# Kernel optimization log

Hardware: AMD Instinct MI355X
Metric: run time of the kernel (lower is better)

## Reference

```python
import jax, jax.numpy as jnp
import numpy as np

HEAD_DIM = 64
EPS = 1e-06


def yat_dense(x, kernel, bias):
    # YatDense (nmn): y = (x.W)^2 / (||x - w||^2 + eps) * alpha_scale + b
    dot = x @ kernel                                  # [..., F]
    x_sq = jnp.sum(x * x, axis=-1, keepdims=True)     # [..., 1]
    w_sq = jnp.sum(kernel * kernel, axis=0)           # [F]
    dist = x_sq + w_sq - 2.0 * dot                    # squared euclidean distance
    y = (dot * dot) / (dist + EPS)
    feats = kernel.shape[1]
    scale = np.sqrt(feats) / np.log1p(feats)          # alpha=1 scaling
    return y * jnp.asarray(scale, x.dtype) + bias


def apply_rope(q, k):
    # q,k: [B,H,T,D]; interleaved-pair rotation, base 10000 (dim=HEAD_DIM)
    B, H, T, D = q.shape
    half = D // 2
    pos = jnp.arange(T, dtype=jnp.float32)
    freqs = 10000.0 ** (-jnp.arange(half, dtype=jnp.float32) / half)
    ang = pos[:, None] * freqs[None, :]               # [T, half]
    sin = jnp.sin(ang)[None, None, :, :, None]        # [1,1,T,half,1]
    cos = jnp.cos(ang)[None, None, :, :, None]

    def rot(t):
        ts = t.reshape(B, H, T, half, 2)
        t0, t1 = ts[..., 0:1], ts[..., 1:2]
        out = jnp.concatenate([t0 * cos - t1 * sin, t1 * cos + t0 * sin], axis=-1)
        return out.reshape(B, H, T, D)

    return rot(q), rot(k)


def setup_inputs() -> dict:
    key = jax.random.key(0)
    B, T, C, H = 2, 2048, 1024, 16
    k1, k2, k3, k4, k5 = jax.random.split(key, 5)
    x = jax.random.normal(k1, (B, T, C), dtype=jnp.float32)
    # causal mask, broadcast over batch
    mask = jnp.broadcast_to(jnp.tril(jnp.ones((T, T), dtype=bool))[None], (B, T, T))
    s = 1.0 / np.sqrt(C)
    w_attn = jax.random.normal(k2, (C, 3 * C), dtype=jnp.float32) * s
    b_attn = jnp.zeros((3 * C,), dtype=jnp.float32)
    w_proj = jax.random.normal(k3, (C, C), dtype=jnp.float32) * s
    b_proj = jnp.zeros((C,), dtype=jnp.float32)
    return {"x": x, "mask": mask, "w_attn": w_attn, "b_attn": b_attn,
            "w_proj": w_proj, "b_proj": b_proj}


def reference(x, mask, w_attn, b_attn, w_proj, b_proj):
    B, T, C = x.shape
    H = C // HEAD_DIM
    qkv = yat_dense(x, w_attn, b_attn)                     # [B,T,3C]
    qkv = qkv.reshape(B, T, 3, H, HEAD_DIM)
    q, k, v = jnp.moveaxis(qkv, 2, 0)                      # each [B,T,H,hd]
    q = jnp.swapaxes(q, 1, 2)                              # [B,H,T,hd]
    k = jnp.swapaxes(k, 1, 2)
    v = jnp.swapaxes(v, 1, 2)
    q, k = apply_rope(q, k)
    scale = jnp.asarray(np.sqrt(HEAD_DIM), x.dtype)
    attn = jnp.einsum('bhqd,bhkd->bhqk', q, k) / scale     # [B,H,T,T]
    neg = jnp.finfo(x.dtype).min
    attn = jnp.where(mask[:, None, :, :], attn, neg)
    attn = jax.nn.softmax(attn, axis=-1)
    out = jnp.einsum('bhqk,bhkd->bhqd', attn, v)           # [B,H,T,hd]
    out = jnp.swapaxes(out, 1, 2).reshape(B, T, C)
    return yat_dense(out, w_proj, b_proj)
```

## Files before the change

### kernel.cpp

```cpp
#include <hip/hip_runtime.h>
#include <hip/hip_bf16.h>
#include <cmath>

#define BB 2
#define TT 2048
#define CC 1024
#define HH 16
#define DD 64
#define ROWS (BB*TT)
#define N1 (3*CC)
#define EPS 1e-6f

using short8 = __attribute__((ext_vector_type(8))) short;
using f32x4  = __attribute__((ext_vector_type(4))) float;

__device__ __forceinline__ void gl_lds16(const __hip_bfloat16* g, unsigned short* l) {
    __builtin_amdgcn_global_load_lds(
        (const __attribute__((address_space(1))) unsigned int*)(g),
        (__attribute__((address_space(3))) unsigned int*)(l), 16, 0, 0);
}

__device__ __forceinline__ unsigned int bf16pair(float a, float b) {
    __hip_bfloat16 ha = (__hip_bfloat16)a, hb = (__hip_bfloat16)b;
    unsigned short ua = *(unsigned short*)&ha, ub = *(unsigned short*)&hb;
    return (unsigned int)ua | ((unsigned int)ub << 16);
}

__global__ void rope_rowsq(const float* __restrict__ X, float* __restrict__ xsq,
                           __hip_bfloat16* __restrict__ Xb, float* __restrict__ osq,
                           float* __restrict__ rope,
                           float* __restrict__ wsqa, float* __restrict__ wsqp) {
    int blk = blockIdx.x;
    int t = threadIdx.x;
    if (blk >= ROWS) {
        int idx = (blk - ROWS) * 256 + t;
        if (idx < N1) wsqa[idx] = 0.f;
        if (idx < CC) wsqp[idx] = 0.f;
        if (idx < TT * 32) {
            int tt = idx >> 5, i = idx & 31;
            double freq = pow(10000.0, -(double)i / 32.0);
            float ang = (float)tt * (float)freq;
            rope[idx * 2 + 0] = cosf(ang);
            rope[idx * 2 + 1] = sinf(ang);
        }
        return;
    }
    int row = blk;
    const float* xr = X + (size_t)row * CC;
    __hip_bfloat16* br = Xb + (size_t)row * CC;
    float p = 0.f;
#pragma unroll
    for (int i = 0; i < 4; ++i) {
        float v = xr[t + i * 256];
        p += v * v;
        br[t + i * 256] = (__hip_bfloat16)v;
    }
    __shared__ float s[256];
    s[t] = p;
    __syncthreads();
    for (int off = 128; off > 0; off >>= 1) {
        if (t < off) s[t] += s[t + off];
        __syncthreads();
    }
    if (t == 0) { xsq[row] = s[0]; osq[row] = 0.f; }
}

__global__ void transpose2(const float* __restrict__ Wa, __hip_bfloat16* __restrict__ WaT,
                           float* __restrict__ wsqa,
                           const float* __restrict__ Wp, __hip_bfloat16* __restrict__ WpT,
                           float* __restrict__ wsqp) {
    const float* W; __hip_bfloat16* Wt; float* wsq; int N;
    if (blockIdx.z == 0) { W = Wa; Wt = WaT; wsq = wsqa; N = N1; }
    else { if (blockIdx.x >= 16) return; W = Wp; Wt = WpT; wsq = wsqp; N = CC; }
    const int K = CC;
    __shared__ unsigned short tile[64][65];
    int n0 = blockIdx.x * 64, k0 = blockIdx.y * 64;
    int c = threadIdx.x & 63, rg = threadIdx.x >> 6;
    float part = 0.f;
#pragma unroll
    for (int rr = 0; rr < 16; ++rr) {
        int r = rg + rr * 4;
        float f = W[(size_t)(k0 + r) * N + n0 + c];
        __hip_bfloat16 h = (__hip_bfloat16)f;
        tile[r][c] = *(unsigned short*)&h;
        part += f * f;
    }
    atomicAdd(&wsq[n0 + c], part);
    __syncthreads();
#pragma unroll
    for (int rr = 0; rr < 16; ++rr) {
        int r = rg + rr * 4;
        unsigned short u = tile[c][r];
        Wt[(size_t)(n0 + r) * K + k0 + c] = *(__hip_bfloat16*)&u;
    }
}

__global__ __launch_bounds__(256) void yat_gemm_qkv(
    const __hip_bfloat16* __restrict__ A,
    const __hip_bfloat16* __restrict__ Bt,
    const float* __restrict__ xsq, const float* __restrict__ wsq,
    const float* __restrict__ bias, const float* __restrict__ rope,
    __hip_bfloat16* __restrict__ Qb, __hip_bfloat16* __restrict__ Kb,
    __hip_bfloat16* __restrict__ Vb, float scale) {
    const int K = CC, N = N1;
    __shared__ __align__(16) unsigned short As0[128 * 32], As1[128 * 32];
    __shared__ __align__(16) unsigned short Bs0[128 * 32], Bs1[128 * 32];
    int tid = threadIdx.x;
    int wave = tid >> 6, lane = tid & 63, quad = lane >> 4, l16 = lane & 15;
    int wr = wave >> 1, wc = wave & 1;
    int m0 = blockIdx.y * 128, n0 = blockIdx.x * 128;

    f32x4 acc[4][4];
#pragma unroll
    for (int mt = 0; mt < 4; ++mt)
#pragma unroll
        for (int nt = 0; nt < 4; ++nt) acc[mt][nt] = f32x4{0.f, 0.f, 0.f, 0.f};

    int srow = lane >> 2, soff = (lane & 3) << 3;
    for (int k0 = 0; k0 < K; k0 += 64) {
        __syncthreads();
#pragma unroll
        for (int i = 0; i < 2; ++i) {
            int rowc = (wave * 2 + i) * 16;
            const __hip_bfloat16* ap = A + (size_t)(m0 + rowc + srow) * K + k0 + soff;
            gl_lds16(ap,      As0 + rowc * 32);
            gl_lds16(ap + 32, As1 + rowc * 32);
            const __hip_bfloat16* bp = Bt + (size_t)(n0 + rowc + srow) * K + k0 + soff;
            gl_lds16(bp,      Bs0 + rowc * 32);
            gl_lds16(bp + 32, Bs1 + rowc * 32);
        }
        __syncthreads();
#pragma unroll
        for (int h = 0; h < 2; ++h) {
            const unsigned short* Ah = h ? As1 : As0;
            const unsigned short* Bh = h ? Bs1 : Bs0;
            short8 af[4], bf[4];
#pragma unroll
            for (int mt = 0; mt < 4; ++mt)
                af[mt] = *(const short8*)(Ah + (wr * 64 + mt * 16 + l16) * 32 + quad * 8);
#pragma unroll
            for (int nt = 0; nt < 4; ++nt)
                bf[nt] = *(const short8*)(Bh + (wc * 64 + nt * 16 + l16) * 32 + quad * 8);
#pragma unroll
            for (int mt = 0; mt < 4; ++mt)
#pragma unroll
                for (int nt = 0; nt < 4; ++nt)
                    acc[mt][nt] = __builtin_amdgcn_mfma_f32_16x16x32_bf16(af[mt], bf[nt], acc[mt][nt], 0, 0, 0);
        }
    }
    const float QSC = 0.125f * 1.44269504f;
    int mb = m0 + wr * 64 + quad * 4;
    int cbase = n0 + wc * 64;
    int sec = n0 >> 10;
    if (sec == 2) {
#pragma unroll
        for (int nt = 0; nt < 4; ++nt) {
            int col = cbase + nt * 16 + l16;
            float wq = wsq[col], bs = bias[col];
            int h = (col & 1023) >> 6, d = col & 63;
#pragma unroll
            for (int mt = 0; mt < 4; ++mt) {
#pragma unroll
                for (int r = 0; r < 4; ++r) {
                    int row = mb + mt * 16 + r;
                    float dot = acc[mt][nt][r];
                    float dist = xsq[row] + wq - 2.f * dot + EPS;
                    float y = dot * dot / dist * scale + bs;
                    int t = row & (TT - 1), bI = row >> 11;
                    Vb[(((size_t)bI * HH + h) * TT + t) * DD + d] = (__hip_bfloat16)y;
                }
            }
        }
    } else {
        __hip_bfloat16* dst = sec ? Kb : Qb;
        float sc = sec ? 1.f : QSC;
#pragma unroll
        for (int nt = 0; nt < 4; ++nt) {
            int col = cbase + nt * 16 + l16;
            float wq = wsq[col], bs = bias[col];
            int h = (col & 1023) >> 6, d = col & 63;
            int odd = l16 & 1;
#pragma unroll
            for (int mt = 0; mt < 4; ++mt) {
#pragma unroll
                for (int r = 0; r < 4; ++r) {
                    int row = mb + mt * 16 + r;
                    float dot = acc[mt][nt][r];
                    float dist = xsq[row] + wq - 2.f * dot + EPS;
                    float y = dot * dot / dist * scale + bs;
                    float yp = __shfl_xor(y, 1, 64);
                    int t = row & (TT - 1), bI = row >> 11;
                    const float* rp = rope + (size_t)t * 64 + (d & 62);
                    float cs = rp[0] * sc, sn = rp[1] * sc;
                    float o = odd ? (y * cs + yp * sn) : (y * cs - yp * sn);
                    dst[(((size_t)bI * HH + h) * TT + t) * DD + d] = (__hip_bfloat16)o;
                }
            }
        }
    }
}

__global__ __launch_bounds__(256) void vtrans(const unsigned short* __restrict__ Vb,
                                              __hip_bfloat16* __restrict__ Vtb) {
    int bh = blockIdx.y, t0 = blockIdx.x * 64, tid = threadIdx.x;
    __shared__ unsigned short vt[64][72];
    int r = tid >> 2, g = (tid & 3) * 16;
    const unsigned short* src = Vb + ((size_t)bh * TT + t0 + r) * DD + g;
    *(uint4*)&vt[r][g]     = *(const uint4*)src;
    *(uint4*)&vt[r][g + 8] = *(const uint4*)(src + 8);
    __syncthreads();
    union U8 { uint4 v; unsigned short s[8]; };
#pragma unroll
    for (int p = 0; p < 2; ++p) {
        int d = (tid >> 3) + p * 32, tl = (tid & 7) * 8;
        U8 w;
#pragma unroll
        for (int j = 0; j < 8; ++j) w.s[j] = vt[tl + j][d];
        *(uint4*)(Vtb + ((size_t)bh * DD + d) * TT + t0 + tl) = w.v;
    }
}

__global__ __launch_bounds__(256, 3) void attn_mfma6(
    const __hip_bfloat16* __restrict__ Qb, const __hip_bfloat16* __restrict__ Kb,
    const __hip_bfloat16* __restrict__ Vtb,
    __hip_bfloat16* __restrict__ out, float* __restrict__ osq) {
    int i = blockIdx.x;
    int xcd = i & 7;
    int r0 = i >> 3;
    int bh = xcd + 8 * (r0 & 3);
    int rr = r0 >> 2;
    int v = rr & 7, s2 = rr >> 3;
    int qblk = (s2 == 0) ? v : (s2 == 1) ? (15 - v) : (s2 == 2) ? (16 + v) : (31 - v);
    int b = bh >> 4, h = bh & 15;
    int tid = threadIdx.x;
    int wave = tid >> 6, lane = tid & 63, quad = lane >> 4, l16 = lane & 15;

    __shared__ __align__(16) unsigned short Ks[2][64 * 32];
    __shared__ __align__(16) unsigned short Vs[2][64 * 32];
    __shared__ __align__(16) unsigned short Ps[4][16 * 72];
    unsigned short* pp = &Ps[wave][0];

    const __hip_bfloat16* Qbase = Qb + (size_t)bh * TT * DD;
    const __hip_bfloat16* Kbase = Kb + (size_t)bh * TT * DD;
    const __hip_bfloat16* Vbase = Vtb + (size_t)bh * DD * TT;

    int qw = qblk * 64 + wave * 16;
    short8 qf0, qf1;
    {
        const __hip_bfloat16* qr = Qbase + (size_t)(qw + l16) * DD + quad * 8;
        qf0 = *(const short8*)(qr);
        qf1 = *(const short8*)(qr + 32);
    }
    short8 ones8;
#pragma unroll
    for (int u = 0; u < 8; ++u) ones8[u] = (short)0x3F80;

    f32x4 acc_o[4];
#pragma unroll
    for (int mt = 0; mt < 4; ++mt) acc_o[mt] = f32x4{0.f, 0.f, 0.f, 0.f};
    f32x4 acc_l = {0.f, 0.f, 0.f, 0.f};

    int srow = lane >> 2;
    int soff = (lane & 3) * 8;
    int q_g = qw + l16;

    for (int kt = 0; kt <= qblk; ++kt) {
        int k0 = kt * 64;
        __syncthreads();
        gl_lds16(Kbase + (size_t)(k0 + wave * 16 + srow) * DD + soff,      &Ks[0][wave * 512]);
        gl_lds16(Kbase + (size_t)(k0 + wave * 16 + srow) * DD + 32 + soff, &Ks[1][wave * 512]);
        gl_lds16(Vbase + (size_t)(wave * 16 + srow) * TT + k0 + soff,      &Vs[0][wave * 512]);
        gl_lds16(Vbase + (size_t)(wave * 16 + srow) * TT + k0 + 32 + soff, &Vs[1][wave * 512]);
        __syncthreads();

        f32x4 accs[4];
#pragma unroll
        for (int mt = 0; mt < 4; ++mt) {
            short8 kf0 = *(const short8*)(&Ks[0][(mt * 16 + l16) * 32 + quad * 8]);
            short8 kf1 = *(const short8*)(&Ks[1][(mt * 16 + l16) * 32 + quad * 8]);
            f32x4 z = {0.f, 0.f, 0.f, 0.f};
            z = __builtin_amdgcn_mfma_f32_16x16x32_bf16(kf0, qf0, z, 0, 0, 0);
            accs[mt] = __builtin_amdgcn_mfma_f32_16x16x32_bf16(kf1, qf1, z, 0, 0, 0);
        }
        int limit = (kt == qblk) ? q_g : 0x7FFFFFFF;
#pragma unroll
        for (int mt = 0; mt < 4; ++mt) {
            int keyb = k0 + mt * 16 + quad * 4;
            float p0 = exp2f(accs[mt][0]);
            float p1 = exp2f(accs[mt][1]);
            float p2 = exp2f(accs[mt][2]);
            float p3 = exp2f(accs[mt][3]);
            p0 = (keyb + 0 <= limit) ? p0 : 0.f;
            p1 = (keyb + 1 <= limit) ? p1 : 0.f;
            p2 = (keyb + 2 <= limit) ? p2 : 0.f;
            p3 = (keyb + 3 <= limit) ? p3 : 0.f;
            uint2 w2;
            w2.x = bf16pair(p0, p1);
            w2.y = bf16pair(p2, p3);
            *(uint2*)(pp + l16 * 72 + mt * 16 + quad * 4) = w2;
        }
        short8 pf0 = *(const short8*)(pp + l16 * 72 + quad * 8);
        short8 pf1 = *(const short8*)(pp + l16 * 72 + 32 + quad * 8);
#pragma unroll
        for (int mt = 0; mt < 4; ++mt) {
            short8 vf0 = *(const short8*)(&Vs[0][(mt * 16 + l16) * 32 + quad * 8]);
            short8 vf1 = *(const short8*)(&Vs[1][(mt * 16 + l16) * 32 + quad * 8]);
            acc_o[mt] = __builtin_amdgcn_mfma_f32_16x16x32_bf16(vf0, pf0, acc_o[mt], 0, 0, 0);
            acc_o[mt] = __builtin_amdgcn_mfma_f32_16x16x32_bf16(vf1, pf1, acc_o[mt], 0, 0, 0);
        }
        acc_l = __builtin_amdgcn_mfma_f32_16x16x32_bf16(ones8, pf0, acc_l, 0, 0, 0);
        acc_l = __builtin_amdgcn_mfma_f32_16x16x32_bf16(ones8, pf1, acc_l, 0, 0, 0);
    }
    float inv = 1.f / acc_l[0];
    float part = 0.f;
#pragma unroll
    for (int mt = 0; mt < 4; ++mt) {
        float o0 = acc_o[mt][0] * inv;
        float o1 = acc_o[mt][1] * inv;
        float o2 = acc_o[mt][2] * inv;
        float o3 = acc_o[mt][3] * inv;
        part += o0 * o0 + o1 * o1 + o2 * o2 + o3 * o3;
        uint2 w2;
        w2.x = bf16pair(o0, o1);
        w2.y = bf16pair(o2, o3);
        *(uint2*)(pp + l16 * 72 + mt * 16 + quad * 4) = w2;
    }
    part += __shfl_xor(part, 16, 64);
    part += __shfl_xor(part, 32, 64);
    if (quad == 0) atomicAdd(&osq[(size_t)b * TT + qw + l16], part);
    int rw = lane >> 2, cg = lane & 3;
    uint4 o0 = *(const uint4*)(pp + rw * 72 + cg * 16);
    uint4 o1 = *(const uint4*)(pp + rw * 72 + cg * 16 + 8);
    __hip_bfloat16* orow = out + (size_t)(b * TT + qw + rw) * CC + h * DD + cg * 16;
    *(uint4*)(orow) = o0;
    *(uint4*)(orow + 8) = o1;
}

template<int TM, int TN, typename OutT>
__global__ __launch_bounds__(256) void yat_gemm_bk64(
    const __hip_bfloat16* __restrict__ A,
    const __hip_bfloat16* __restrict__ Bt,
    const float* __restrict__ xsq, const float* __restrict__ wsq,
    const float* __restrict__ bias, OutT* __restrict__ C,
    int M, int N, int K, float scale) {
    constexpr int MT = TM / 32;
    constexpr int NT = TN / 32;
    constexpr int IA = TM / 64;
    constexpr int IB = TN / 64;
    __shared__ __align__(16) unsigned short As0[TM * 32];
    __shared__ __align__(16) unsigned short As1[TM * 32];
    __shared__ __align__(16) unsigned short Bs0[TN * 32];
    __shared__ __align__(16) unsigned short Bs1[TN * 32];
    int tid = threadIdx.x;
    int wave = tid >> 6, lane = tid & 63, quad = lane >> 4, l16 = lane & 15;
    int wr = wave >> 1, wc = wave & 1;
    int m0 = blockIdx.y * TM, n0 = blockIdx.x * TN;

    f32x4 acc[MT][NT];
#pragma unroll
    for (int mt = 0; mt < MT; ++mt)
#pragma unroll
        for (int nt = 0; nt < NT; ++nt) acc[mt][nt] = f32x4{0.f, 0.f, 0.f, 0.f};

    int srow = lane >> 2, soff = (lane & 3) << 3;
    for (int k0 = 0; k0 < K; k0 += 64) {
        __syncthreads();
#pragma unroll
        for (int i = 0; i < IA; ++i) {
            int rowc = (wave * IA + i) * 16;
            const __hip_bfloat16* ap = A + (size_t)(m0 + rowc + srow) * K + k0 + soff;
            gl_lds16(ap,      As0 + rowc * 32);
            gl_lds16(ap + 32, As1 + rowc * 32);
        }
#pragma unroll
        for (int i = 0; i < IB; ++i) {
            int rowc = (wave * IB + i) * 16;
            const __hip_bfloat16* bp = Bt + (size_t)(n0 + rowc + srow) * K + k0 + soff;
            gl_lds16(bp,      Bs0 + rowc * 32);
            gl_lds16(bp + 32, Bs1 + rowc * 32);
        }
        __syncthreads();
#pragma unroll
        for (int h = 0; h < 2; ++h) {
            const unsigned short* Ah = h ? As1 : As0;
            const unsigned short* Bh = h ? Bs1 : Bs0;
            short8 af[MT], bf[NT];
#pragma unroll
            for (int mt = 0; mt < MT; ++mt)
                af[mt] = *(const short8*)(Ah + (wr * (TM / 2) + mt * 16 + l16) * 32 + quad * 8);
#pragma unroll
            for (int nt = 0; nt < NT; ++nt)
                bf[nt] = *(const short8*)(Bh + (wc * (TN / 2) + nt * 16 + l16) * 32 + quad * 8);
#pragma unroll
            for (int mt = 0; mt < MT; ++mt)
#pragma unroll
                for (int nt = 0; nt < NT; ++nt)
                    acc[mt][nt] = __builtin_amdgcn_mfma_f32_16x16x32_bf16(af[mt], bf[nt], acc[mt][nt], 0, 0, 0);
        }
    }
    int mb = m0 + wr * (TM / 2) + quad * 4;
#pragma unroll
    for (int nt = 0; nt < NT; ++nt) {
        int col = n0 + wc * (TN / 2) + nt * 16 + l16;
        float wq = wsq[col];
        float bs = bias[col];
#pragma unroll
        for (int mt = 0; mt < MT; ++mt) {
#pragma unroll
            for (int r = 0; r < 4; ++r) {
                int row = mb + mt * 16 + r;
                float dot = acc[mt][nt][r];
                float dist = xsq[row] + wq - 2.f * dot + EPS;
                C[(size_t)row * N + col] = (OutT)(dot * dot / dist * scale + bs);
            }
        }
    }
}

extern "C" void kernel_launch(void* const* d_in, const int* in_sizes, int n_in,
                              void* d_out, int out_size, void* d_ws, size_t ws_size,
                              hipStream_t stream) {
    const float* x      = (const float*)d_in[0];
    const float* w_attn = (const float*)d_in[2];
    const float* b_attn = (const float*)d_in[3];
    const float* w_proj = (const float*)d_in[4];
    const float* b_proj = (const float*)d_in[5];
    float* out = (float*)d_out;

    char* ws = (char*)d_ws;
    __hip_bfloat16* xbf  = (__hip_bfloat16*)(ws + 0);
    __hip_bfloat16* aout = (__hip_bfloat16*)(ws + 8388608);
    __hip_bfloat16* watT = (__hip_bfloat16*)(ws + 16777216);
    __hip_bfloat16* wpT  = (__hip_bfloat16*)(ws + 23068672);
    float*          rope = (float*)(ws + 25165824);
    float*          xsq  = (float*)(ws + 25690112);
    float*          osq  = (float*)(ws + 25706496);
    float*          wsqa = (float*)(ws + 25722880);
    float*          wsqp = (float*)(ws + 25735168);
    __hip_bfloat16* Qb   = (__hip_bfloat16*)(ws + 25739264);
    __hip_bfloat16* Kb   = (__hip_bfloat16*)(ws + 34127872);
    __hip_bfloat16* Vb   = (__hip_bfloat16*)(ws + 42516480);
    __hip_bfloat16* Vtb  = (__hip_bfloat16*)(ws + 50905088);

    float scale1 = (float)(sqrt(3072.0) / log1p(3072.0));
    float scale2 = (float)(sqrt(1024.0) / log1p(1024.0));

    rope_rowsq<<<ROWS + 256, 256, 0, stream>>>(x, xsq, xbf, osq, rope, wsqa, wsqp);
    transpose2<<<dim3(48, 16, 2), 256, 0, stream>>>(w_attn, watT, wsqa, w_proj, wpT, wsqp);
    yat_gemm_qkv<<<dim3(N1 / 128, ROWS / 128), 256, 0, stream>>>(
        xbf, watT, xsq, wsqa, b_attn, rope, Qb, Kb, Vb, scale1);
    vtrans<<<dim3(TT / 64, BB * HH), 256, 0, stream>>>((const unsigned short*)Vb, Vtb);
    attn_mfma6<<<1024, 256, 0, stream>>>(Qb, Kb, Vtb, aout, osq);
    yat_gemm_bk64<128, 64, float><<<dim3(CC / 64, ROWS / 128), 256, 0, stream>>>(
        aout, wpT, osq, wsqp, b_proj, out, ROWS, CC, CC, scale2);
}
```

Baseline: 246.8 us.

## Double-buffer attention K/V, pair causal blocks, move RoPE out of QKV GEMM

The attention kernel now double-buffers its K/V LDS tiles so the next tile's loads overlap the current tile's MFMAs. Causal query blocks are paired per workgroup (768 blocks) to balance work. RoPE is moved out of the QKV GEMM epilogue: K is rotated in place in the V-transpose kernel and Q is rotated when loaded in attention. The row-norm reduction switches to wave shuffles, and the output projection uses smaller 64x64 tiles. The cost is extra K read/write traffic, more LDS per block, and a different occupancy and scheduling balance.

```diff
diff --git a/kernel.cpp b/kernel.cpp
--- a/kernel.cpp
+++ b/kernel.cpp
@@ -26,10 +26,15 @@
     return (unsigned int)ua | ((unsigned int)ub << 16);
 }
 
-__global__ void rope_rowsq(const float* __restrict__ X, float* __restrict__ xsq,
-                           __hip_bfloat16* __restrict__ Xb, float* __restrict__ osq,
-                           float* __restrict__ rope,
-                           float* __restrict__ wsqa, float* __restrict__ wsqp) {
+__device__ __forceinline__ float bf2f(unsigned short u) {
+    unsigned int v = (unsigned int)u << 16;
+    return *(float*)&v;
+}
+
+__global__ void aux_rowsq(const float* __restrict__ X, float* __restrict__ xsq,
+                          __hip_bfloat16* __restrict__ Xb, float* __restrict__ osq,
+                          float* __restrict__ rope,
+                          float* __restrict__ wsqa, float* __restrict__ wsqp) {
     int blk = blockIdx.x;
     int t = threadIdx.x;
     if (blk >= ROWS) {
@@ -55,14 +60,12 @@
         p += v * v;
         br[t + i * 256] = (__hip_bfloat16)v;
     }
-    __shared__ float s[256];
-    s[t] = p;
+#pragma unroll
+    for (int off = 32; off > 0; off >>= 1) p += __shfl_xor(p, off, 64);
+    __shared__ float s4[4];
+    if ((t & 63) == 0) s4[t >> 6] = p;
     __syncthreads();
-    for (int off = 128; off > 0; off >>= 1) {
-        if (t < off) s[t] += s[t + off];
-        __syncthreads();
-    }
-    if (t == 0) { xsq[row] = s[0]; osq[row] = 0.f; }
+    if (t == 0) { xsq[row] = s4[0] + s4[1] + s4[2] + s4[3]; osq[row] = 0.f; }
 }
 
 __global__ void transpose2(const float* __restrict__ Wa, __hip_bfloat16* __restrict__ WaT,
@@ -95,14 +98,14 @@
     }
 }
 
-__global__ __launch_bounds__(256) void yat_gemm_qkv(
+__global__ __launch_bounds__(256) void yat_gemm_qkv2(
     const __hip_bfloat16* __restrict__ A,
     const __hip_bfloat16* __restrict__ Bt,
     const float* __restrict__ xsq, const float* __restrict__ wsq,
-    const float* __restrict__ bias, const float* __restrict__ rope,
+    const float* __restrict__ bias,
     __hip_bfloat16* __restrict__ Qb, __hip_bfloat16* __restrict__ Kb,
     __hip_bfloat16* __restrict__ Vb, float scale) {
-    const int K = CC, N = N1;
+    const int K = CC;
     __shared__ __align__(16) unsigned short As0[128 * 32], As1[128 * 32];
     __shared__ __align__(16) unsigned short Bs0[128 * 32], Bs1[128 * 32];
     int tid = threadIdx.x;
@@ -148,95 +151,84 @@
                     acc[mt][nt] = __builtin_amdgcn_mfma_f32_16x16x32_bf16(af[mt], bf[nt], acc[mt][nt], 0, 0, 0);
         }
     }
-    const float QSC = 0.125f * 1.44269504f;
     int mb = m0 + wr * 64 + quad * 4;
-    int cbase = n0 + wc * 64;
-    int sec = n0 >> 10;
-    if (sec == 2) {
-#pragma unroll
-        for (int nt = 0; nt < 4; ++nt) {
-            int col = cbase + nt * 16 + l16;
-            float wq = wsq[col], bs = bias[col];
-            int h = (col & 1023) >> 6, d = col & 63;
-#pragma unroll
-            for (int mt = 0; mt < 4; ++mt) {
-#pragma unroll
-                for (int r = 0; r < 4; ++r) {
-                    int row = mb + mt * 16 + r;
-                    float dot = acc[mt][nt][r];
-                    float dist = xsq[row] + wq - 2.f * dot + EPS;
-                    float y = dot * dot / dist * scale + bs;
-                    int t = row & (TT - 1), bI = row >> 11;
-                    Vb[(((size_t)bI * HH + h) * TT + t) * DD + d] = (__hip_bfloat16)y;
-                }
-            }
-        }
-    } else {
-        __hip_bfloat16* dst = sec ? Kb : Qb;
-        float sc = sec ? 1.f : QSC;
-#pragma unroll
-        for (int nt = 0; nt < 4; ++nt) {
-            int col = cbase + nt * 16 + l16;
-            float wq = wsq[col], bs = bias[col];
-            int h = (col & 1023) >> 6, d = col & 63;
-            int odd = l16 & 1;
-#pragma unroll
-            for (int mt = 0; mt < 4; ++mt) {
-#pragma unroll
-                for (int r = 0; r < 4; ++r) {
-                    int row = mb + mt * 16 + r;
-                    float dot = acc[mt][nt][r];
-                    float dist = xsq[row] + wq - 2.f * dot + EPS;
-                    float y = dot * dot / dist * scale + bs;
-                    float yp = __shfl_xor(y, 1, 64);
-                    int t = row & (TT - 1), bI = row >> 11;
-                    const float* rp = rope + (size_t)t * 64 + (d & 62);
-                    float cs = rp[0] * sc, sn = rp[1] * sc;
-                    float o = odd ? (y * cs + yp * sn) : (y * cs - yp * sn);
-                    dst[(((size_t)bI * HH + h) * TT + t) * DD + d] = (__hip_bfloat16)o;
-                }
-            }
-        }
-    }
-}
-
-__global__ __launch_bounds__(256) void vtrans(const unsigned short* __restrict__ Vb,
-                                              __hip_bfloat16* __restrict__ Vtb) {
+#pragma unroll
+    for (int nt = 0; nt < 4; ++nt) {
+        int col = n0 + wc * 64 + nt * 16 + l16;
+        float wq = wsq[col], bs = bias[col];
+        int sec = col >> 10, cc2 = col & 1023;
+        int h = cc2 >> 6, d = cc2 & 63;
+        __hip_bfloat16* dst = (sec == 0) ? Qb : ((sec == 1) ? Kb : Vb);
+#pragma unroll
+        for (int mt = 0; mt < 4; ++mt) {
+#pragma unroll
+            for (int r = 0; r < 4; ++r) {
+                int row = mb + mt * 16 + r;
+                float dot = acc[mt][nt][r];
+                float dist = xsq[row] + wq - 2.f * dot + EPS;
+                float y = dot * dot / dist * scale + bs;
+                int t = row & (TT - 1), bI = row >> 11;
+                dst[(((size_t)bI * HH + h) * TT + t) * DD + d] = (__hip_bfloat16)y;
+            }
+        }
+    }
+}
+
+__global__ __launch_bounds__(256) void ropek_vtrans(
+    unsigned short* __restrict__ Kb, const unsigned short* __restrict__ Vb,
+    __hip_bfloat16* __restrict__ Vtb, const float* __restrict__ rope) {
     int bh = blockIdx.y, t0 = blockIdx.x * 64, tid = threadIdx.x;
     __shared__ unsigned short vt[64][72];
-    int r = tid >> 2, g = (tid & 3) * 16;
-    const unsigned short* src = Vb + ((size_t)bh * TT + t0 + r) * DD + g;
-    *(uint4*)&vt[r][g]     = *(const uint4*)src;
-    *(uint4*)&vt[r][g + 8] = *(const uint4*)(src + 8);
+    int r = tid >> 2, g = tid & 3;
+    const unsigned short* src = Vb + ((size_t)bh * TT + t0 + r) * DD + g * 16;
+    *(uint4*)&vt[r][g * 16]     = *(const uint4*)src;
+    *(uint4*)&vt[r][g * 16 + 8] = *(const uint4*)(src + 8);
+    {
+        int t = t0 + r;
+        unsigned short* kp = Kb + ((size_t)bh * TT + t) * DD + g * 16;
+        union U8 { uint4 v; unsigned short s[8]; } k0v, k1v, o0, o1;
+        k0v.v = *(const uint4*)kp;
+        k1v.v = *(const uint4*)(kp + 8);
+        const float* rp = rope + (size_t)t * 64 + g * 16;
+#pragma unroll
+        for (int u = 0; u < 8; ++u) {
+            float c = rp[2 * u], sn = rp[2 * u + 1];
+            unsigned short ev = (u < 4) ? k0v.s[2 * u]     : k1v.s[2 * u - 8];
+            unsigned short ov = (u < 4) ? k0v.s[2 * u + 1] : k1v.s[2 * u - 7];
+            float f0 = bf2f(ev), f1 = bf2f(ov);
+            unsigned int pr = bf16pair(f0 * c - f1 * sn, f1 * c + f0 * sn);
+            if (u < 4) ((unsigned int*)&o0)[u] = pr;
+            else       ((unsigned int*)&o1)[u - 4] = pr;
+        }
+        *(uint4*)kp = o0.v;
+        *(uint4*)(kp + 8) = o1.v;
+    }
     __syncthreads();
-    union U8 { uint4 v; unsigned short s[8]; };
+    union U8b { uint4 v; unsigned short s[8]; };
 #pragma unroll
     for (int p = 0; p < 2; ++p) {
         int d = (tid >> 3) + p * 32, tl = (tid & 7) * 8;
-        U8 w;
+        U8b w;
 #pragma unroll
         for (int j = 0; j < 8; ++j) w.s[j] = vt[tl + j][d];
         *(uint4*)(Vtb + ((size_t)bh * DD + d) * TT + t0 + tl) = w.v;
     }
 }
 
-__global__ __launch_bounds__(256, 3) void attn_mfma6(
+__global__ __launch_bounds__(256, 3) void attn_mfma8(
     const __hip_bfloat16* __restrict__ Qb, const __hip_bfloat16* __restrict__ Kb,
-    const __hip_bfloat16* __restrict__ Vtb,
+    const __hip_bfloat16* __restrict__ Vtb, const float* __restrict__ rope,
     __hip_bfloat16* __restrict__ out, float* __restrict__ osq) {
+    const float QSC = 0.125f * 1.44269504f;
     int i = blockIdx.x;
-    int xcd = i & 7;
-    int r0 = i >> 3;
-    int bh = xcd + 8 * (r0 & 3);
-    int rr = r0 >> 2;
-    int v = rr & 7, s2 = rr >> 3;
-    int qblk = (s2 == 0) ? v : (s2 == 1) ? (15 - v) : (s2 == 2) ? (16 + v) : (31 - v);
+    int xcd = i & 7, jj = (i >> 3) & 3, s = i >> 5;
+    int bh = xcd + 8 * jj;
     int b = bh >> 4, h = bh & 15;
     int tid = threadIdx.x;
     int wave = tid >> 6, lane = tid & 63, quad = lane >> 4, l16 = lane & 15;
 
-    __shared__ __align__(16) unsigned short Ks[2][64 * 32];
-    __shared__ __align__(16) unsigned short Vs[2][64 * 32];
+    __shared__ __align__(16) unsigned short Ks[2][2][64 * 32];
+    __shared__ __align__(16) unsigned short Vs[2][2][64 * 32];
     __shared__ __align__(16) unsigned short Ps[4][16 * 72];
     unsigned short* pp = &Ps[wave][0];
 
@@ -244,96 +236,125 @@
     const __hip_bfloat16* Kbase = Kb + (size_t)bh * TT * DD;
     const __hip_bfloat16* Vbase = Vtb + (size_t)bh * DD * TT;
 
-    int qw = qblk * 64 + wave * 16;
-    short8 qf0, qf1;
-    {
-        const __hip_bfloat16* qr = Qbase + (size_t)(qw + l16) * DD + quad * 8;
-        qf0 = *(const short8*)(qr);
-        qf1 = *(const short8*)(qr + 32);
-    }
+    int srow = lane >> 2, soff = (lane & 3) * 8;
     short8 ones8;
 #pragma unroll
     for (int u = 0; u < 8; ++u) ones8[u] = (short)0x3F80;
 
-    f32x4 acc_o[4];
-#pragma unroll
-    for (int mt = 0; mt < 4; ++mt) acc_o[mt] = f32x4{0.f, 0.f, 0.f, 0.f};
-    f32x4 acc_l = {0.f, 0.f, 0.f, 0.f};
-
-    int srow = lane >> 2;
-    int soff = (lane & 3) * 8;
-    int q_g = qw + l16;
-
-    for (int kt = 0; kt <= qblk; ++kt) {
-        int k0 = kt * 64;
+    int u0, u1, nunits;
+    if (s < 8)       { u0 = s;      u1 = 15 - s; nunits = 2; }
+    else if (s < 16) { u0 = s + 8;  u1 = 0;      nunits = 1; }
+    else             { u0 = 47 - s; u1 = 0;      nunits = 1; }
+
+    for (int un = 0; un < nunits; ++un) {
+        int qblk = un ? u1 : u0;
+        int qw = qblk * 64 + wave * 16;
+        short8 qf0, qf1;
+        {
+            int t = qw + l16;
+            const unsigned short* qr = (const unsigned short*)(Qbase + (size_t)t * DD) + quad * 8;
+            union S8 { short8 v; unsigned short s[8]; } r0, r1, o0v, o1v;
+            r0.v = *(const short8*)qr;
+            r1.v = *(const short8*)(qr + 32);
+            const float* rpa = rope + (size_t)t * 64 + quad * 8;
+            const float* rpb = rpa + 32;
+#pragma unroll
+            for (int u = 0; u < 4; ++u) {
+                float c = rpa[2 * u] * QSC, sn = rpa[2 * u + 1] * QSC;
+                float e = bf2f(r0.s[2 * u]), o = bf2f(r0.s[2 * u + 1]);
+                ((unsigned int*)&o0v)[u] = bf16pair(e * c - o * sn, o * c + e * sn);
+                float c2 = rpb[2 * u] * QSC, sn2 = rpb[2 * u + 1] * QSC;
+                float e2 = bf2f(r1.s[2 * u]), o2 = bf2f(r1.s[2 * u + 1]);
+                ((unsigned int*)&o1v)[u] = bf16pair(e2 * c2 - o2 * sn2, o2 * c2 + e2 * sn2);
+            }
+            qf0 = o0v.v;
+            qf1 = o1v.v;
+        }
+        f32x4 acc_o[4];
+#pragma unroll
+        for (int mt = 0; mt < 4; ++mt) acc_o[mt] = f32x4{0.f, 0.f, 0.f, 0.f};
+        f32x4 acc_l = {0.f, 0.f, 0.f, 0.f};
+        int q_g = qw + l16;
+
         __syncthreads();
-        gl_lds16(Kbase + (size_t)(k0 + wave * 16 + srow) * DD + soff,      &Ks[0][wave * 512]);
-        gl_lds16(Kbase + (size_t)(k0 + wave * 16 + srow) * DD + 32 + soff, &Ks[1][wave * 512]);
-        gl_lds16(Vbase + (size_t)(wave * 16 + srow) * TT + k0 + soff,      &Vs[0][wave * 512]);
-        gl_lds16(Vbase + (size_t)(wave * 16 + srow) * TT + k0 + 32 + soff, &Vs[1][wave * 512]);
-        __syncthreads();
-
-        f32x4 accs[4];
+        gl_lds16(Kbase + (size_t)(wave * 16 + srow) * DD + soff,      &Ks[0][0][wave * 512]);
+        gl_lds16(Kbase + (size_t)(wave * 16 + srow) * DD + 32 + soff, &Ks[0][1][wave * 512]);
+        gl_lds16(Vbase + (size_t)(wave * 16 + srow) * TT + soff,      &Vs[0][0][wave * 512]);
+        gl_lds16(Vbase + (size_t)(wave * 16 + srow) * TT + 32 + soff, &Vs[0][1][wave * 512]);
+
+        for (int kt = 0; kt <= qblk; ++kt) {
+            int cur = kt & 1;
+            int k0 = kt * 64;
+            __syncthreads();
+            if (kt < qblk) {
+                int nb = cur ^ 1, kn = k0 + 64;
+                gl_lds16(Kbase + (size_t)(kn + wave * 16 + srow) * DD + soff,      &Ks[nb][0][wave * 512]);
+                gl_lds16(Kbase + (size_t)(kn + wave * 16 + srow) * DD + 32 + soff, &Ks[nb][1][wave * 512]);
+                gl_lds16(Vbase + (size_t)(wave * 16 + srow) * TT + kn + soff,      &Vs[nb][0][wave * 512]);
+                gl_lds16(Vbase + (size_t)(wave * 16 + srow) * TT + kn + 32 + soff, &Vs[nb][1][wave * 512]);
+            }
+            f32x4 accs[4];
+#pragma unroll
+            for (int mt = 0; mt < 4; ++mt) {
+                short8 kf0 = *(const short8*)(&Ks[cur][0][(mt * 16 + l16) * 32 + quad * 8]);
+                short8 kf1 = *(const short8*)(&Ks[cur][1][(mt * 16 + l16) * 32 + quad * 8]);
+                f32x4 z = {0.f, 0.f, 0.f, 0.f};
+                z = __builtin_amdgcn_mfma_f32_16x16x32_bf16(kf0, qf0, z, 0, 0, 0);
+                accs[mt] = __builtin_amdgcn_mfma_f32_16x16x32_bf16(kf1, qf1, z, 0, 0, 0);
+            }
+            int limit = (kt == qblk) ? q_g : 0x7FFFFFFF;
+#pragma unroll
+            for (int mt = 0; mt < 4; ++mt) {
+                int keyb = k0 + mt * 16 + quad * 4;
+                float p0 = exp2f(accs[mt][0]);
+                float p1 = exp2f(accs[mt][1]);
+                float p2 = exp2f(accs[mt][2]);
+                float p3 = exp2f(accs[mt][3]);
+                p0 = (keyb + 0 <= limit) ? p0 : 0.f;
+                p1 = (keyb + 1 <= limit) ? p1 : 0.f;
+                p2 = (keyb + 2 <= limit) ? p2 : 0.f;
+                p3 = (keyb + 3 <= limit) ? p3 : 0.f;
+                uint2 w2;
+                w2.x = bf16pair(p0, p1);
+                w2.y = bf16pair(p2, p3);
+                *(uint2*)(pp + l16 * 72 + mt * 16 + quad * 4) = w2;
+            }
+            short8 pf0 = *(const short8*)(pp + l16 * 72 + quad * 8);
+            short8 pf1 = *(const short8*)(pp + l16 * 72 + 32 + quad * 8);
+#pragma unroll
+            for (int mt = 0; mt < 4; ++mt) {
+                short8 vf0 = *(const short8*)(&Vs[cur][0][(mt * 16 + l16) * 32 + quad * 8]);
+                short8 vf1 = *(const short8*)(&Vs[cur][1][(mt * 16 + l16) * 32 + quad * 8]);
+                acc_o[mt] = __builtin_amdgcn_mfma_f32_16x16x32_bf16(vf0, pf0, acc_o[mt], 0, 0, 0);
+                acc_o[mt] = __builtin_amdgcn_mfma_f32_16x16x32_bf16(vf1, pf1, acc_o[mt], 0, 0, 0);
+            }
+            acc_l = __builtin_amdgcn_mfma_f32_16x16x32_bf16(ones8, pf0, acc_l, 0, 0, 0);
+            acc_l = __builtin_amdgcn_mfma_f32_16x16x32_bf16(ones8, pf1, acc_l, 0, 0, 0);
+        }
+        float inv = 1.f / acc_l[0];
+        float part = 0.f;
 #pragma unroll
         for (int mt = 0; mt < 4; ++mt) {
-            short8 kf0 = *(const short8*)(&Ks[0][(mt * 16 + l16) * 32 + quad * 8]);
-            short8 kf1 = *(const short8*)(&Ks[1][(mt * 16 + l16) * 32 + quad * 8]);
-            f32x4 z = {0.f, 0.f, 0.f, 0.f};
-            z = __builtin_amdgcn_mfma_f32_16x16x32_bf16(kf0, qf0, z, 0, 0, 0);
-            accs[mt] = __builtin_amdgcn_mfma_f32_16x16x32_bf16(kf1, qf1, z, 0, 0, 0);
-        }
-        int limit = (kt == qblk) ? q_g : 0x7FFFFFFF;
-#pragma unroll
-        for (int mt = 0; mt < 4; ++mt) {
-            int keyb = k0 + mt * 16 + quad * 4;
-            float p0 = exp2f(accs[mt][0]);
-            float p1 = exp2f(accs[mt][1]);
-            float p2 = exp2f(accs[mt][2]);
-            float p3 = exp2f(accs[mt][3]);
-            p0 = (keyb + 0 <= limit) ? p0 : 0.f;
-            p1 = (keyb + 1 <= limit) ? p1 : 0.f;
-            p2 = (keyb + 2 <= limit) ? p2 : 0.f;
-            p3 = (keyb + 3 <= limit) ? p3 : 0.f;
+            float o0 = acc_o[mt][0] * inv;
+            float o1 = acc_o[mt][1] * inv;
+            float o2 = acc_o[mt][2] * inv;
+            float o3 = acc_o[mt][3] * inv;
+            part += o0 * o0 + o1 * o1 + o2 * o2 + o3 * o3;
             uint2 w2;
-            w2.x = bf16pair(p0, p1);
-            w2.y = bf16pair(p2, p3);
+            w2.x = bf16pair(o0, o1);
+            w2.y = bf16pair(o2, o3);
             *(uint2*)(pp + l16 * 72 + mt * 16 + quad * 4) = w2;
         }
-        short8 pf0 = *(const short8*)(pp + l16 * 72 + quad * 8);
-        short8 pf1 = *(const short8*)(pp + l16 * 72 + 32 + quad * 8);
-#pragma unroll
-        for (int mt = 0; mt < 4; ++mt) {
-            short8 vf0 = *(const short8*)(&Vs[0][(mt * 16 + l16) * 32 + quad * 8]);
-            short8 vf1 = *(const short8*)(&Vs[1][(mt * 16 + l16) * 32 + quad * 8]);
-            acc_o[mt] = __builtin_amdgcn_mfma_f32_16x16x32_bf16(vf0, pf0, acc_o[mt], 0, 0, 0);
-            acc_o[mt] = __builtin_amdgcn_mfma_f32_16x16x32_bf16(vf1, pf1, acc_o[mt], 0, 0, 0);
-        }
-        acc_l = __builtin_amdgcn_mfma_f32_16x16x32_bf16(ones8, pf0, acc_l, 0, 0, 0);
-        acc_l = __builtin_amdgcn_mfma_f32_16x16x32_bf16(ones8, pf1, acc_l, 0, 0, 0);
-    }
-    float inv = 1.f / acc_l[0];
-    float part = 0.f;
-#pragma unroll
-    for (int mt = 0; mt < 4; ++mt) {
-        float o0 = acc_o[mt][0] * inv;
-        float o1 = acc_o[mt][1] * inv;
-        float o2 = acc_o[mt][2] * inv;
-        float o3 = acc_o[mt][3] * inv;
-        part += o0 * o0 + o1 * o1 + o2 * o2 + o3 * o3;
-        uint2 w2;
-        w2.x = bf16pair(o0, o1);
-        w2.y = bf16pair(o2, o3);
-        *(uint2*)(pp + l16 * 72 + mt * 16 + quad * 4) = w2;
-    }
-    part += __shfl_xor(part, 16, 64);
-    part += __shfl_xor(part, 32, 64);
-    if (quad == 0) atomicAdd(&osq[(size_t)b * TT + qw + l16], part);
-    int rw = lane >> 2, cg = lane & 3;
-    uint4 o0 = *(const uint4*)(pp + rw * 72 + cg * 16);
-    uint4 o1 = *(const uint4*)(pp + rw * 72 + cg * 16 + 8);
-    __hip_bfloat16* orow = out + (size_t)(b * TT + qw + rw) * CC + h * DD + cg * 16;
-    *(uint4*)(orow) = o0;
-    *(uint4*)(orow + 8) = o1;
+        part += __shfl_xor(part, 16, 64);
+        part += __shfl_xor(part, 32, 64);
+        if (quad == 0) atomicAdd(&osq[(size_t)b * TT + qw + l16], part);
+        int rw = lane >> 2, cg = lane & 3;
+        uint4 o0 = *(const uint4*)(pp + rw * 72 + cg * 16);
+        uint4 o1 = *(const uint4*)(pp + rw * 72 + cg * 16 + 8);
+        __hip_bfloat16* orow = out + (size_t)(b * TT + qw + rw) * CC + h * DD + cg * 16;
+        *(uint4*)(orow) = o0;
+        *(uint4*)(orow + 8) = o1;
+    }
 }
 
 template<int TM, int TN, typename OutT>
@@ -445,12 +466,13 @@
     float scale1 = (float)(sqrt(3072.0) / log1p(3072.0));
     float scale2 = (float)(sqrt(1024.0) / log1p(1024.0));
 
-    rope_rowsq<<<ROWS + 256, 256, 0, stream>>>(x, xsq, xbf, osq, rope, wsqa, wsqp);
+    aux_rowsq<<<ROWS + 256, 256, 0, stream>>>(x, xsq, xbf, osq, rope, wsqa, wsqp);
     transpose2<<<dim3(48, 16, 2), 256, 0, stream>>>(w_attn, watT, wsqa, w_proj, wpT, wsqp);
-    yat_gemm_qkv<<<dim3(N1 / 128, ROWS / 128), 256, 0, stream>>>(
-        xbf, watT, xsq, wsqa, b_attn, rope, Qb, Kb, Vb, scale1);
-    vtrans<<<dim3(TT / 64, BB * HH), 256, 0, stream>>>((const unsigned short*)Vb, Vtb);
-    attn_mfma6<<<1024, 256, 0, stream>>>(Qb, Kb, Vtb, aout, osq);
-    yat_gemm_bk64<128, 64, float><<<dim3(CC / 64, ROWS / 128), 256, 0, stream>>>(
+    yat_gemm_qkv2<<<dim3(N1 / 128, ROWS / 128), 256, 0, stream>>>(
+        xbf, watT, xsq, wsqa, b_attn, Qb, Kb, Vb, scale1);
+    ropek_vtrans<<<dim3(TT / 64, BB * HH), 256, 0, stream>>>(
+        (unsigned short*)Kb, (const unsigned short*)Vb, Vtb, rope);
+    attn_mfma8<<<768, 256, 0, stream>>>(Qb, Kb, Vtb, rope, aout, osq);
+    yat_gemm_bk64<64, 64, float><<<dim3(CC / 64, ROWS / 64), 256, 0, stream>>>(
         aout, wpT, osq, wsqp, b_proj, out, ROWS, CC, CC, scale2);
 }
```

After: 220.6 us. 10.6% less time.
